# Kernel tuning notes

Measured on AMD Instinct MI355X. Metric: run time of the kernel, lower is better.

## Reference

```python
import jax, jax.numpy as jnp
import numpy as np

H = 8        # num_heads
LN_EPS = 1e-5
NEG = -1000000.0


def setup_inputs() -> dict:
    key = jax.random.key(0)
    ks = jax.random.split(key, 8)
    B, T, D = 4, 4096, 1024
    s = 1.0 / np.sqrt(D)
    x = jax.random.normal(ks[0], (B, T, D), dtype=jnp.float32)
    tmask = (jnp.arange(T) < (3 * T) // 4).astype(jnp.float32)
    src_mask = jnp.broadcast_to(tmask[None, :, None], (B, T, 1)).astype(jnp.float32)
    Wq = jax.random.normal(ks[1], (D, D), dtype=jnp.float32) * s
    Wk = jax.random.normal(ks[2], (D, D), dtype=jnp.float32) * s
    Wv = jax.random.normal(ks[3], (D, D), dtype=jnp.float32) * s
    bq = jnp.zeros((D,), jnp.float32)
    bk = jnp.zeros((D,), jnp.float32)
    bv = jnp.zeros((D,), jnp.float32)
    gamma = jnp.ones((D,), jnp.float32)
    beta = jnp.zeros((D,), jnp.float32)
    return {"x": x, "src_mask": src_mask, "Wq": Wq, "bq": bq, "Wk": Wk,
            "bk": bk, "Wv": Wv, "bv": bv, "gamma": gamma, "beta": beta}


def reference(x, src_mask, Wq, bq, Wk, bk, Wv, bv, gamma, beta):
    B, T, D = x.shape
    Dh = D // H
    # LayerNorm (same normed input feeds q, k, v)
    mu = jnp.mean(x, axis=-1, keepdims=True)
    var = jnp.mean(jnp.square(x - mu), axis=-1, keepdims=True)
    xn = (x - mu) * jax.lax.rsqrt(var + LN_EPS) * gamma + beta
    q = xn @ Wq + bq                               # [B,T,D]
    k = xn @ Wk + bk + (1.0 - src_mask) * NEG      # mask padded timesteps
    v = (xn @ Wv + bv) * src_mask                  # zero padded values
    q = jax.nn.softmax(q.reshape(B, T, H, Dh), axis=-1)   # over feature dim
    k = jax.nn.softmax(k.reshape(B, T, H, Dh), axis=1)    # over time dim
    v = v.reshape(B, T, H, Dh)
    # efficient/linear attention: O(T * Dh^2) per head
    att = jnp.einsum('bnhd,bnhl->bhdl', k, v)      # [B,H,Dh,Dh]
    y = jnp.einsum('bnhd,bhdl->bnhl', q, att).reshape(B, T, D)
    return x + y
```

## Files before the change

### kernel.cpp

```cpp
#include <hip/hip_runtime.h>
#include <stdint.h>


typedef unsigned short u16;
typedef __attribute__((ext_vector_type(8))) short bf16x8;
typedef __attribute__((ext_vector_type(4))) float f32x4;

__device__ u16 g_WT[3][1024 * 1024];
__device__ u16 g_xn[16777216];
__device__ u16 g_ekT[16777216];
__device__ u16 g_vvT[16777216];
__device__ float g_attp[8388608];
__device__ u16 g_attT[524288];
__device__ float g_Z[4096];

__device__ __forceinline__ float b2f(u16 u) {
  union { unsigned int i; float f; } c;
  c.i = ((unsigned int)u) << 16;
  return c.f;
}
__device__ __forceinline__ u16 f2b(float f) {
  union { float f; unsigned int i; } c;
  c.f = f;
  unsigned int r = c.i + 0x7fffu + ((c.i >> 16) & 1u);
  return (u16)(r >> 16);
}

__device__ __forceinline__ void gload16(const void* g, void* l) {
  __builtin_amdgcn_global_load_lds(
      reinterpret_cast<const __attribute__((address_space(1))) uint32_t*>(
          reinterpret_cast<uintptr_t>(g)),
      reinterpret_cast<__attribute__((address_space(3))) uint32_t*>(
          reinterpret_cast<uintptr_t>(l)),
      16, 0, 0);
}

__device__ __forceinline__ void stage128x32(const u16* g, int stride, char* lds,
                                            int wave, int lane) {
  const int r = wave * 32 + (lane >> 2);
  const int cb = (lane & 3) * 16;
  const char* gp = (const char*)g;
  gload16(gp + (size_t)r * stride * 2 + cb, lds + wave * 2048);
  gload16(gp + (size_t)(r + 16) * stride * 2 + cb, lds + wave * 2048 + 1024);
}

__device__ __forceinline__ bf16x8 frag_ld(const char* lds, int row, int lane) {
  return *(const bf16x8*)(lds + row * 64 + ((lane >> 4) * 16));
}

__global__ __launch_bounds__(256) void ln_kernel(const float* __restrict__ x,
                                                 const float* __restrict__ gamma,
                                                 const float* __restrict__ beta) {
  const int row = blockIdx.x;
  const int tid = threadIdx.x;
  const int wave = tid >> 6, lane = tid & 63;
  const float* xr = x + (size_t)row * 1024;
  float4 u = ((const float4*)xr)[tid];
  float v0 = u.x, v1 = u.y, v2 = u.z, v3 = u.w;
  float s = v0 + v1 + v2 + v3;
  float s2 = v0 * v0 + v1 * v1 + v2 * v2 + v3 * v3;
#pragma unroll
  for (int off = 32; off > 0; off >>= 1) {
    s += __shfl_down(s, off);
    s2 += __shfl_down(s2, off);
  }
  __shared__ float ls[4], ls2[4];
  if (lane == 0) { ls[wave] = s; ls2[wave] = s2; }
  __syncthreads();
  s = ls[0] + ls[1] + ls[2] + ls[3];
  s2 = ls2[0] + ls2[1] + ls2[2] + ls2[3];
  const float mu = s * (1.0f / 1024.0f);
  const float var = fmaxf(s2 * (1.0f / 1024.0f) - mu * mu, 0.0f);
  const float rstd = rsqrtf(var + 1e-5f);
  float4 g4 = ((const float4*)gamma)[tid];
  float4 be = ((const float4*)beta)[tid];
  ushort4 o;
  o.x = f2b((v0 - mu) * rstd * g4.x + be.x);
  o.y = f2b((v1 - mu) * rstd * g4.y + be.y);
  o.z = f2b((v2 - mu) * rstd * g4.z + be.z);
  o.w = f2b((v3 - mu) * rstd * g4.w + be.w);
  *(ushort4*)(g_xn + (size_t)row * 1024 + tid * 4) = o;
}

__global__ __launch_bounds__(256) void transpose_kernel(const float* __restrict__ wq,
                                                        const float* __restrict__ wk,
                                                        const float* __restrict__ wv) {
  __shared__ u16 tile[32][33];
  const int which = blockIdx.z;
  const float* src = (which == 0) ? wq : (which == 1) ? wk : wv;
  u16* dst = g_WT[which];
  const int tx = threadIdx.x & 31;
  const int ty = threadIdx.x >> 5;
  const int c0 = blockIdx.x * 32, r0 = blockIdx.y * 32;
#pragma unroll
  for (int i = 0; i < 4; i++)
    tile[ty + i * 8][tx] = f2b(src[(size_t)(r0 + ty + i * 8) * 1024 + c0 + tx]);
  __syncthreads();
#pragma unroll
  for (int i = 0; i < 4; i++)
    dst[(size_t)(c0 + ty + i * 8) * 1024 + r0 + tx] = tile[tx][ty + i * 8];
}

__global__ __launch_bounds__(256) void gemm_kv(const float* __restrict__ bk,
                                               const float* __restrict__ bv,
                                               const float* __restrict__ mask) {
  __shared__ __align__(16) char smem[34816];
  char* As = smem;
  char* Bs = smem + 8192;
  u16* tT = (u16*)smem;
  const int tid = threadIdx.x, wave = tid >> 6, lane = tid & 63;
  const int L = blockIdx.x;
  const int c = L & 7;
  const int k = L >> 3;
  const int inner = k & 15;
  const int n0 = (inner & 7) * 128;
  const int z = inner >> 3;
  const int m0 = (c + 8 * (k >> 4)) * 128;
  const u16* wt = z ? g_WT[2] : g_WT[1];
  const float* bias = z ? bv : bk;
  u16* outT = z ? g_vvT : g_ekT;
  const int b = m0 >> 12;
  const int t0 = m0 & 4095;
  const int wm = wave & 1, wn = wave >> 1;

  f32x4 zero = {0.f, 0.f, 0.f, 0.f};
  f32x4 acc[4][4];
#pragma unroll
  for (int i = 0; i < 4; i++)
#pragma unroll
    for (int j = 0; j < 4; j++) acc[i][j] = zero;

  for (int k0 = 0; k0 < 1024; k0 += 32) {
    __syncthreads();
    stage128x32(g_xn + (size_t)m0 * 1024 + k0, 1024, As, wave, lane);
    stage128x32(wt + (size_t)n0 * 1024 + k0, 1024, Bs, wave, lane);
    __syncthreads();
    bf16x8 af[4], bfr[4];
#pragma unroll
    for (int i = 0; i < 4; i++) af[i] = frag_ld(As, wm * 64 + i * 16 + (lane & 15), lane);
#pragma unroll
    for (int j = 0; j < 4; j++) bfr[j] = frag_ld(Bs, wn * 64 + j * 16 + (lane & 15), lane);
#pragma unroll
    for (int i = 0; i < 4; i++)
#pragma unroll
      for (int j = 0; j < 4; j++)
        acc[i][j] = __builtin_amdgcn_mfma_f32_16x16x32_bf16(af[i], bfr[j], acc[i][j], 0, 0, 0);
  }
  __syncthreads();

#pragma unroll
  for (int i = 0; i < 4; i++)
#pragma unroll
    for (int r = 0; r < 4; r++) {
      const int rowl = wm * 64 + i * 16 + (lane >> 4) * 4 + r;
      const float mv = mask[m0 + rowl];
#pragma unroll
      for (int j = 0; j < 4; j++) {
        const int coll = wn * 64 + j * 16 + (lane & 15);
        const float a = acc[i][j][r] + bias[n0 + coll];
        float o;
        if (z)
          o = a * mv;
        else
          o = (mv > 0.5f) ? __expf(fminf(a, 30.0f)) : 0.0f;
        tT[coll * 136 + rowl] = f2b(o);
      }
    }
  __syncthreads();
  const size_t gbase = (size_t)b * (1024 * 4096) + (size_t)n0 * 4096 + t0;
#pragma unroll
  for (int u = 0; u < 8; u++) {
    const int v = u * 256 + tid;
    const int cc = v >> 4, rb = (v & 15) * 8;
    uint4 val = *(const uint4*)&tT[cc * 136 + rb];
    *(uint4*)(outT + gbase + (size_t)cc * 4096 + rb) = val;
  }
}

__global__ __launch_bounds__(256) void zrow_kernel() {
  const int tid = threadIdx.x, wave = tid >> 6, lane = tid & 63;
  const int d = blockIdx.x * 4 + wave;
  const int b = blockIdx.y;
  const u16* p = g_ekT + (size_t)b * (1024 * 4096) + (size_t)d * 4096;
  float s = 0.f;
#pragma unroll
  for (int pass = 0; pass < 8; pass++) {
    uint4 w4 = *(const uint4*)(p + pass * 512 + lane * 8);
    unsigned int w[4] = {w4.x, w4.y, w4.z, w4.w};
#pragma unroll
    for (int q = 0; q < 4; q++) {
      s += b2f((u16)(w[q] & 0xffff));
      s += b2f((u16)(w[q] >> 16));
    }
  }
#pragma unroll
  for (int m = 1; m < 64; m <<= 1) s += __shfl_xor(s, m);
  if (lane == 0) g_Z[b * 1024 + d] = s;
}

__global__ __launch_bounds__(256) void gemm_att() {
  __shared__ __align__(16) char As[8192];
  __shared__ __align__(16) char Bs[8192];
  const int tid = threadIdx.x, wave = tid >> 6, lane = tid & 63;
  const int kc = blockIdx.x;
  const int bh = blockIdx.y;
  const int b = bh >> 3, h = bh & 7;
  const size_t base = (size_t)b * (1024 * 4096) + (size_t)(h * 128) * 4096;
  const int wm = wave & 1, wn = wave >> 1;

  f32x4 zero = {0.f, 0.f, 0.f, 0.f};
  f32x4 acc[4][4];
#pragma unroll
  for (int i = 0; i < 4; i++)
#pragma unroll
    for (int j = 0; j < 4; j++) acc[i][j] = zero;

  for (int kt = 0; kt < 256; kt += 32) {
    const int k0 = kc * 256 + kt;
    __syncthreads();
    stage128x32(g_ekT + base + k0, 4096, As, wave, lane);
    stage128x32(g_vvT + base + k0, 4096, Bs, wave, lane);
    __syncthreads();
    bf16x8 af[4], bfr[4];
#pragma unroll
    for (int i = 0; i < 4; i++) af[i] = frag_ld(As, wm * 64 + i * 16 + (lane & 15), lane);
#pragma unroll
    for (int j = 0; j < 4; j++) bfr[j] = frag_ld(Bs, wn * 64 + j * 16 + (lane & 15), lane);
#pragma unroll
    for (int i = 0; i < 4; i++)
#pragma unroll
      for (int j = 0; j < 4; j++)
        acc[i][j] = __builtin_amdgcn_mfma_f32_16x16x32_bf16(af[i], bfr[j], acc[i][j], 0, 0, 0);
  }

  float* op = g_attp + ((size_t)(kc * 32 + bh)) * 16384;
#pragma unroll
  for (int i = 0; i < 4; i++)
#pragma unroll
    for (int r = 0; r < 4; r++) {
      const int row = wm * 64 + i * 16 + (lane >> 4) * 4 + r;
#pragma unroll
      for (int j = 0; j < 4; j++) {
        const int col = wn * 64 + j * 16 + (lane & 15);
        op[row * 128 + col] = acc[i][j][r];
      }
    }
}

__global__ __launch_bounds__(256) void attnorm_kernel() {
  const int bh = blockIdx.x;
  const int b = bh >> 3, h = bh & 7;
  const int tid = threadIdx.x;
  __shared__ float Zl[128];
  if (tid < 128) Zl[tid] = fmaxf(g_Z[b * 1024 + h * 128 + tid], 1e-30f);
  __syncthreads();
  const int i0 = blockIdx.y * 2048;
  for (int i = i0 + tid; i < i0 + 2048; i += 256) {
    const int d = i >> 7, l = i & 127;
    float s = 0.f;
#pragma unroll
    for (int c = 0; c < 16; c++) s += g_attp[((size_t)(c * 32 + bh)) * 16384 + i];
    g_attT[(size_t)bh * 16384 + l * 128 + d] = f2b(s / Zl[d]);
  }
}

__global__ __launch_bounds__(256) void gemm_qy(const float* __restrict__ bq,
                                               const float* __restrict__ x,
                                               float* __restrict__ out) {
  __shared__ __align__(16) char As[8192];
  __shared__ __align__(16) char Bs[8192];
  __shared__ __align__(16) u16 qs[128 * 136];
  __shared__ float zqp[2][128];
  const int tid = threadIdx.x, wave = tid >> 6, lane = tid & 63;
  const int L = blockIdx.x;
  const int c = L & 7;
  const int k = L >> 3;
  const int h = k & 7;
  const int m0 = (c + 8 * (k >> 3)) * 128;
  const int b = m0 >> 12;
  const int bh = b * 8 + h;
  const int wm = wave & 1, wn = wave >> 1;

  f32x4 zero = {0.f, 0.f, 0.f, 0.f};
  f32x4 acc[4][4];
#pragma unroll
  for (int i = 0; i < 4; i++)
#pragma unroll
    for (int j = 0; j < 4; j++) acc[i][j] = zero;

  for (int k0 = 0; k0 < 1024; k0 += 32) {
    __syncthreads();
    stage128x32(g_xn + (size_t)m0 * 1024 + k0, 1024, As, wave, lane);
    stage128x32(g_WT[0] + (size_t)(h * 128) * 1024 + k0, 1024, Bs, wave, lane);
    __syncthreads();
    bf16x8 af[4], bfr[4];
#pragma unroll
    for (int i = 0; i < 4; i++) af[i] = frag_ld(As, wm * 64 + i * 16 + (lane & 15), lane);
#pragma unroll
    for (int j = 0; j < 4; j++) bfr[j] = frag_ld(Bs, wn * 64 + j * 16 + (lane & 15), lane);
#pragma unroll
    for (int i = 0; i < 4; i++)
#pragma unroll
      for (int j = 0; j < 4; j++)
        acc[i][j] = __builtin_amdgcn_mfma_f32_16x16x32_bf16(af[i], bfr[j], acc[i][j], 0, 0, 0);
  }

#pragma unroll
  for (int i = 0; i < 4; i++)
#pragma unroll
    for (int r = 0; r < 4; r++) {
      const int rowl = wm * 64 + i * 16 + (lane >> 4) * 4 + r;
      float rs = 0.f;
#pragma unroll
      for (int j = 0; j < 4; j++) {
        const int coll = wn * 64 + j * 16 + (lane & 15);
        const float e = __expf(fminf(acc[i][j][r] + bq[h * 128 + coll], 30.0f));
        qs[rowl * 136 + coll] = f2b(e);
        rs += e;
      }
      rs += __shfl_xor(rs, 1);
      rs += __shfl_xor(rs, 2);
      rs += __shfl_xor(rs, 4);
      rs += __shfl_xor(rs, 8);
      if ((lane & 15) == 0) zqp[wn][rowl] = rs;
    }
  __syncthreads();

  f32x4 acc2[4][4];
#pragma unroll
  for (int i = 0; i < 4; i++)
#pragma unroll
    for (int j = 0; j < 4; j++) acc2[i][j] = zero;

  for (int k0 = 0; k0 < 128; k0 += 32) {
    __syncthreads();
    stage128x32(g_attT + (size_t)bh * 16384 + k0, 128, Bs, wave, lane);
    __syncthreads();
    bf16x8 af[4], bfr[4];
#pragma unroll
    for (int i = 0; i < 4; i++)
      af[i] = *(const bf16x8*)&qs[(wm * 64 + i * 16 + (lane & 15)) * 136 + k0 + (lane >> 4) * 8];
#pragma unroll
    for (int j = 0; j < 4; j++) bfr[j] = frag_ld(Bs, wn * 64 + j * 16 + (lane & 15), lane);
#pragma unroll
    for (int i = 0; i < 4; i++)
#pragma unroll
      for (int j = 0; j < 4; j++)
        acc2[i][j] = __builtin_amdgcn_mfma_f32_16x16x32_bf16(af[i], bfr[j], acc2[i][j], 0, 0, 0);
  }

#pragma unroll
  for (int i = 0; i < 4; i++)
#pragma unroll
    for (int r = 0; r < 4; r++) {
      const int rowl = wm * 64 + i * 16 + (lane >> 4) * 4 + r;
      const float zq = fmaxf(zqp[0][rowl] + zqp[1][rowl], 1e-30f);
      const size_t n = (size_t)m0 + rowl;
#pragma unroll
      for (int j = 0; j < 4; j++) {
        const int coll = wn * 64 + j * 16 + (lane & 15);
        const size_t idx = n * 1024 + h * 128 + coll;
        out[idx] = x[idx] + acc2[i][j][r] / zq;
      }
    }
}

extern "C" void kernel_launch(void* const* d_in, const int* in_sizes, int n_in,
                              void* d_out, int out_size, void* d_ws, size_t ws_size,
                              hipStream_t stream) {
  const float* x = (const float*)d_in[0];
  const float* mask = (const float*)d_in[1];
  const float* Wq = (const float*)d_in[2];
  const float* bq = (const float*)d_in[3];
  const float* Wk = (const float*)d_in[4];
  const float* bk = (const float*)d_in[5];
  const float* Wv = (const float*)d_in[6];
  const float* bv = (const float*)d_in[7];
  const float* gamma = (const float*)d_in[8];
  const float* beta = (const float*)d_in[9];
  float* out = (float*)d_out;
  (void)d_ws; (void)ws_size;

  transpose_kernel<<<dim3(32, 32, 3), 256, 0, stream>>>(Wq, Wk, Wv);
  ln_kernel<<<dim3(16384), 256, 0, stream>>>(x, gamma, beta);
  gemm_kv<<<dim3(2048), 256, 0, stream>>>(bk, bv, mask);
  zrow_kernel<<<dim3(256, 4), 256, 0, stream>>>();
  gemm_att<<<dim3(16, 32), 256, 0, stream>>>();
  attnorm_kernel<<<dim3(32, 8), 256, 0, stream>>>();
  gemm_qy<<<dim3(1024), 256, 0, stream>>>(bq, x, out);
}
```

Baseline: 380.1 us.

## Double-buffer GEMM LDS staging, merge LN with transpose, fuse Z sums into gemm_kv

```diff
diff --git a/kernel.cpp b/kernel.cpp
--- a/kernel.cpp
+++ b/kernel.cpp
@@ -48,65 +48,86 @@
   return *(const bf16x8*)(lds + row * 64 + ((lane >> 4) * 16));
 }
 
-__global__ __launch_bounds__(256) void ln_kernel(const float* __restrict__ x,
-                                                 const float* __restrict__ gamma,
-                                                 const float* __restrict__ beta) {
-  const int row = blockIdx.x;
+__device__ __forceinline__ void tile_mfma(const char* As, const char* Bs,
+                                          f32x4 (&acc)[4][4], int wm, int wn,
+                                          int lane) {
+  bf16x8 af[4], bfr[4];
+#pragma unroll
+  for (int i = 0; i < 4; i++) af[i] = frag_ld(As, wm * 64 + i * 16 + (lane & 15), lane);
+#pragma unroll
+  for (int j = 0; j < 4; j++) bfr[j] = frag_ld(Bs, wn * 64 + j * 16 + (lane & 15), lane);
+#pragma unroll
+  for (int i = 0; i < 4; i++)
+#pragma unroll
+    for (int j = 0; j < 4; j++)
+      acc[i][j] = __builtin_amdgcn_mfma_f32_16x16x32_bf16(af[i], bfr[j], acc[i][j], 0, 0, 0);
+}
+
+__global__ __launch_bounds__(256) void prep_kernel(const float* __restrict__ x,
+                                                   const float* __restrict__ gamma,
+                                                   const float* __restrict__ beta,
+                                                   const float* __restrict__ wq,
+                                                   const float* __restrict__ wk,
+                                                   const float* __restrict__ wv) {
+  __shared__ float ls[4], ls2[4];
+  __shared__ u16 tile[32][33];
+  const int bid = blockIdx.x;
   const int tid = threadIdx.x;
-  const int wave = tid >> 6, lane = tid & 63;
-  const float* xr = x + (size_t)row * 1024;
-  float4 u = ((const float4*)xr)[tid];
-  float v0 = u.x, v1 = u.y, v2 = u.z, v3 = u.w;
-  float s = v0 + v1 + v2 + v3;
-  float s2 = v0 * v0 + v1 * v1 + v2 * v2 + v3 * v3;
-#pragma unroll
-  for (int off = 32; off > 0; off >>= 1) {
-    s += __shfl_down(s, off);
-    s2 += __shfl_down(s2, off);
-  }
-  __shared__ float ls[4], ls2[4];
-  if (lane == 0) { ls[wave] = s; ls2[wave] = s2; }
-  __syncthreads();
-  s = ls[0] + ls[1] + ls[2] + ls[3];
-  s2 = ls2[0] + ls2[1] + ls2[2] + ls2[3];
-  const float mu = s * (1.0f / 1024.0f);
-  const float var = fmaxf(s2 * (1.0f / 1024.0f) - mu * mu, 0.0f);
-  const float rstd = rsqrtf(var + 1e-5f);
-  float4 g4 = ((const float4*)gamma)[tid];
-  float4 be = ((const float4*)beta)[tid];
-  ushort4 o;
-  o.x = f2b((v0 - mu) * rstd * g4.x + be.x);
-  o.y = f2b((v1 - mu) * rstd * g4.y + be.y);
-  o.z = f2b((v2 - mu) * rstd * g4.z + be.z);
-  o.w = f2b((v3 - mu) * rstd * g4.w + be.w);
-  *(ushort4*)(g_xn + (size_t)row * 1024 + tid * 4) = o;
-}
-
-__global__ __launch_bounds__(256) void transpose_kernel(const float* __restrict__ wq,
-                                                        const float* __restrict__ wk,
-                                                        const float* __restrict__ wv) {
-  __shared__ u16 tile[32][33];
-  const int which = blockIdx.z;
-  const float* src = (which == 0) ? wq : (which == 1) ? wk : wv;
-  u16* dst = g_WT[which];
-  const int tx = threadIdx.x & 31;
-  const int ty = threadIdx.x >> 5;
-  const int c0 = blockIdx.x * 32, r0 = blockIdx.y * 32;
-#pragma unroll
-  for (int i = 0; i < 4; i++)
-    tile[ty + i * 8][tx] = f2b(src[(size_t)(r0 + ty + i * 8) * 1024 + c0 + tx]);
-  __syncthreads();
-#pragma unroll
-  for (int i = 0; i < 4; i++)
-    dst[(size_t)(c0 + ty + i * 8) * 1024 + r0 + tx] = tile[tx][ty + i * 8];
+  if (bid < 16384) {
+    if (bid < 16) g_Z[bid * 256 + tid] = 0.0f;
+    const int wave = tid >> 6, lane = tid & 63;
+    const float* xr = x + (size_t)bid * 1024;
+    float4 u = ((const float4*)xr)[tid];
+    float v0 = u.x, v1 = u.y, v2 = u.z, v3 = u.w;
+    float s = v0 + v1 + v2 + v3;
+    float s2 = v0 * v0 + v1 * v1 + v2 * v2 + v3 * v3;
+#pragma unroll
+    for (int off = 32; off > 0; off >>= 1) {
+      s += __shfl_down(s, off);
+      s2 += __shfl_down(s2, off);
+    }
+    if (lane == 0) { ls[wave] = s; ls2[wave] = s2; }
+    __syncthreads();
+    s = ls[0] + ls[1] + ls[2] + ls[3];
+    s2 = ls2[0] + ls2[1] + ls2[2] + ls2[3];
+    const float mu = s * (1.0f / 1024.0f);
+    const float var = fmaxf(s2 * (1.0f / 1024.0f) - mu * mu, 0.0f);
+    const float rstd = rsqrtf(var + 1e-5f);
+    float4 g4 = ((const float4*)gamma)[tid];
+    float4 be = ((const float4*)beta)[tid];
+    ushort4 o;
+    o.x = f2b((v0 - mu) * rstd * g4.x + be.x);
+    o.y = f2b((v1 - mu) * rstd * g4.y + be.y);
+    o.z = f2b((v2 - mu) * rstd * g4.z + be.z);
+    o.w = f2b((v3 - mu) * rstd * g4.w + be.w);
+    *(ushort4*)(g_xn + (size_t)bid * 1024 + tid * 4) = o;
+  } else {
+    const int id = bid - 16384;
+    const int which = id >> 10;
+    const int rem = id & 1023;
+    const float* src = (which == 0) ? wq : (which == 1) ? wk : wv;
+    u16* dst = g_WT[which];
+    const int tx = tid & 31;
+    const int ty = tid >> 5;
+    const int c0 = (rem & 31) * 32, r0 = (rem >> 5) * 32;
+#pragma unroll
+    for (int i = 0; i < 4; i++)
+      tile[ty + i * 8][tx] = f2b(src[(size_t)(r0 + ty + i * 8) * 1024 + c0 + tx]);
+    __syncthreads();
+#pragma unroll
+    for (int i = 0; i < 4; i++)
+      dst[(size_t)(c0 + ty + i * 8) * 1024 + r0 + tx] = tile[tx][ty + i * 8];
+  }
 }
 
 __global__ __launch_bounds__(256) void gemm_kv(const float* __restrict__ bk,
                                                const float* __restrict__ bv,
                                                const float* __restrict__ mask) {
   __shared__ __align__(16) char smem[34816];
-  char* As = smem;
-  char* Bs = smem + 8192;
+  char* A0 = smem;
+  char* B0 = smem + 8192;
+  char* A1 = smem + 16384;
+  char* B1 = smem + 24576;
   u16* tT = (u16*)smem;
   const int tid = threadIdx.x, wave = tid >> 6, lane = tid & 63;
   const int L = blockIdx.x;
@@ -122,6 +143,8 @@
   const int b = m0 >> 12;
   const int t0 = m0 & 4095;
   const int wm = wave & 1, wn = wave >> 1;
+  const u16* Ag = g_xn + (size_t)m0 * 1024;
+  const u16* Bg = wt + (size_t)n0 * 1024;
 
   f32x4 zero = {0.f, 0.f, 0.f, 0.f};
   f32x4 acc[4][4];
@@ -130,24 +153,23 @@
 #pragma unroll
     for (int j = 0; j < 4; j++) acc[i][j] = zero;
 
-  for (int k0 = 0; k0 < 1024; k0 += 32) {
-    __syncthreads();
-    stage128x32(g_xn + (size_t)m0 * 1024 + k0, 1024, As, wave, lane);
-    stage128x32(wt + (size_t)n0 * 1024 + k0, 1024, Bs, wave, lane);
-    __syncthreads();
-    bf16x8 af[4], bfr[4];
-#pragma unroll
-    for (int i = 0; i < 4; i++) af[i] = frag_ld(As, wm * 64 + i * 16 + (lane & 15), lane);
-#pragma unroll
-    for (int j = 0; j < 4; j++) bfr[j] = frag_ld(Bs, wn * 64 + j * 16 + (lane & 15), lane);
-#pragma unroll
-    for (int i = 0; i < 4; i++)
-#pragma unroll
-      for (int j = 0; j < 4; j++)
-        acc[i][j] = __builtin_amdgcn_mfma_f32_16x16x32_bf16(af[i], bfr[j], acc[i][j], 0, 0, 0);
-  }
-  __syncthreads();
-
+  stage128x32(Ag, 1024, A0, wave, lane);
+  stage128x32(Bg, 1024, B0, wave, lane);
+  __syncthreads();
+  for (int k0 = 0; k0 < 1024; k0 += 64) {
+    stage128x32(Ag + k0 + 32, 1024, A1, wave, lane);
+    stage128x32(Bg + k0 + 32, 1024, B1, wave, lane);
+    tile_mfma(A0, B0, acc, wm, wn, lane);
+    __syncthreads();
+    if (k0 + 64 < 1024) {
+      stage128x32(Ag + k0 + 64, 1024, A0, wave, lane);
+      stage128x32(Bg + k0 + 64, 1024, B0, wave, lane);
+    }
+    tile_mfma(A1, B1, acc, wm, wn, lane);
+    __syncthreads();
+  }
+
+  float fsum[4] = {0.f, 0.f, 0.f, 0.f};
 #pragma unroll
   for (int i = 0; i < 4; i++)
 #pragma unroll
@@ -163,9 +185,20 @@
           o = a * mv;
         else
           o = (mv > 0.5f) ? __expf(fminf(a, 30.0f)) : 0.0f;
-        tT[coll * 136 + rowl] = f2b(o);
+        const u16 ob = f2b(o);
+        tT[coll * 136 + rowl] = ob;
+        if (!z) fsum[j] += b2f(ob);
       }
     }
+  if (!z) {
+#pragma unroll
+    for (int j = 0; j < 4; j++) {
+      float s = fsum[j];
+      s += __shfl_xor(s, 16);
+      s += __shfl_xor(s, 32);
+      if (lane < 16) atomicAdd(&g_Z[b * 1024 + n0 + wn * 64 + j * 16 + lane], s);
+    }
+  }
   __syncthreads();
   const size_t gbase = (size_t)b * (1024 * 4096) + (size_t)n0 * 4096 + t0;
 #pragma unroll
@@ -177,36 +210,20 @@
   }
 }
 
-__global__ __launch_bounds__(256) void zrow_kernel() {
-  const int tid = threadIdx.x, wave = tid >> 6, lane = tid & 63;
-  const int d = blockIdx.x * 4 + wave;
-  const int b = blockIdx.y;
-  const u16* p = g_ekT + (size_t)b * (1024 * 4096) + (size_t)d * 4096;
-  float s = 0.f;
-#pragma unroll
-  for (int pass = 0; pass < 8; pass++) {
-    uint4 w4 = *(const uint4*)(p + pass * 512 + lane * 8);
-    unsigned int w[4] = {w4.x, w4.y, w4.z, w4.w};
-#pragma unroll
-    for (int q = 0; q < 4; q++) {
-      s += b2f((u16)(w[q] & 0xffff));
-      s += b2f((u16)(w[q] >> 16));
-    }
-  }
-#pragma unroll
-  for (int m = 1; m < 64; m <<= 1) s += __shfl_xor(s, m);
-  if (lane == 0) g_Z[b * 1024 + d] = s;
-}
-
 __global__ __launch_bounds__(256) void gemm_att() {
-  __shared__ __align__(16) char As[8192];
-  __shared__ __align__(16) char Bs[8192];
+  __shared__ __align__(16) char smem[32768];
+  char* A0 = smem;
+  char* B0 = smem + 8192;
+  char* A1 = smem + 16384;
+  char* B1 = smem + 24576;
   const int tid = threadIdx.x, wave = tid >> 6, lane = tid & 63;
   const int kc = blockIdx.x;
   const int bh = blockIdx.y;
   const int b = bh >> 3, h = bh & 7;
   const size_t base = (size_t)b * (1024 * 4096) + (size_t)(h * 128) * 4096;
   const int wm = wave & 1, wn = wave >> 1;
+  const u16* Ag = g_ekT + base + kc * 256;
+  const u16* Bg = g_vvT + base + kc * 256;
 
   f32x4 zero = {0.f, 0.f, 0.f, 0.f};
   f32x4 acc[4][4];
@@ -215,22 +232,20 @@
 #pragma unroll
     for (int j = 0; j < 4; j++) acc[i][j] = zero;
 
-  for (int kt = 0; kt < 256; kt += 32) {
-    const int k0 = kc * 256 + kt;
-    __syncthreads();
-    stage128x32(g_ekT + base + k0, 4096, As, wave, lane);
-    stage128x32(g_vvT + base + k0, 4096, Bs, wave, lane);
-    __syncthreads();
-    bf16x8 af[4], bfr[4];
-#pragma unroll
-    for (int i = 0; i < 4; i++) af[i] = frag_ld(As, wm * 64 + i * 16 + (lane & 15), lane);
-#pragma unroll
-    for (int j = 0; j < 4; j++) bfr[j] = frag_ld(Bs, wn * 64 + j * 16 + (lane & 15), lane);
-#pragma unroll
-    for (int i = 0; i < 4; i++)
-#pragma unroll
-      for (int j = 0; j < 4; j++)
-        acc[i][j] = __builtin_amdgcn_mfma_f32_16x16x32_bf16(af[i], bfr[j], acc[i][j], 0, 0, 0);
+  stage128x32(Ag, 4096, A0, wave, lane);
+  stage128x32(Bg, 4096, B0, wave, lane);
+  __syncthreads();
+  for (int kt = 0; kt < 256; kt += 64) {
+    stage128x32(Ag + kt + 32, 4096, A1, wave, lane);
+    stage128x32(Bg + kt + 32, 4096, B1, wave, lane);
+    tile_mfma(A0, B0, acc, wm, wn, lane);
+    __syncthreads();
+    if (kt + 64 < 256) {
+      stage128x32(Ag + kt + 64, 4096, A0, wave, lane);
+      stage128x32(Bg + kt + 64, 4096, B0, wave, lane);
+    }
+    tile_mfma(A1, B1, acc, wm, wn, lane);
+    __syncthreads();
   }
 
   float* op = g_attp + ((size_t)(kc * 32 + bh)) * 16384;
@@ -267,10 +282,15 @@
 __global__ __launch_bounds__(256) void gemm_qy(const float* __restrict__ bq,
                                                const float* __restrict__ x,
                                                float* __restrict__ out) {
-  __shared__ __align__(16) char As[8192];
-  __shared__ __align__(16) char Bs[8192];
-  __shared__ __align__(16) u16 qs[128 * 136];
+  __shared__ __align__(16) char smem[51200];
   __shared__ float zqp[2][128];
+  char* A0 = smem;
+  char* B0 = smem + 8192;
+  char* A1 = smem + 16384;
+  char* B1 = smem + 24576;
+  u16* qs = (u16*)smem;
+  char* C0 = smem + 34816;
+  char* C1 = smem + 43008;
   const int tid = threadIdx.x, wave = tid >> 6, lane = tid & 63;
   const int L = blockIdx.x;
   const int c = L & 7;
@@ -280,6 +300,9 @@
   const int b = m0 >> 12;
   const int bh = b * 8 + h;
   const int wm = wave & 1, wn = wave >> 1;
+  const u16* Ag = g_xn + (size_t)m0 * 1024;
+  const u16* Bg = g_WT[0] + (size_t)(h * 128) * 1024;
+  const u16* Cg = g_attT + (size_t)bh * 16384;
 
   f32x4 zero = {0.f, 0.f, 0.f, 0.f};
   f32x4 acc[4][4];
@@ -288,22 +311,23 @@
 #pragma unroll
     for (int j = 0; j < 4; j++) acc[i][j] = zero;
 
-  for (int k0 = 0; k0 < 1024; k0 += 32) {
-    __syncthreads();
-    stage128x32(g_xn + (size_t)m0 * 1024 + k0, 1024, As, wave, lane);
-    stage128x32(g_WT[0] + (size_t)(h * 128) * 1024 + k0, 1024, Bs, wave, lane);
-    __syncthreads();
-    bf16x8 af[4], bfr[4];
-#pragma unroll
-    for (int i = 0; i < 4; i++) af[i] = frag_ld(As, wm * 64 + i * 16 + (lane & 15), lane);
-#pragma unroll
-    for (int j = 0; j < 4; j++) bfr[j] = frag_ld(Bs, wn * 64 + j * 16 + (lane & 15), lane);
-#pragma unroll
-    for (int i = 0; i < 4; i++)
-#pragma unroll
-      for (int j = 0; j < 4; j++)
-        acc[i][j] = __builtin_amdgcn_mfma_f32_16x16x32_bf16(af[i], bfr[j], acc[i][j], 0, 0, 0);
-  }
+  stage128x32(Ag, 1024, A0, wave, lane);
+  stage128x32(Bg, 1024, B0, wave, lane);
+  __syncthreads();
+  for (int k0 = 0; k0 < 1024; k0 += 64) {
+    stage128x32(Ag + k0 + 32, 1024, A1, wave, lane);
+    stage128x32(Bg + k0 + 32, 1024, B1, wave, lane);
+    tile_mfma(A0, B0, acc, wm, wn, lane);
+    __syncthreads();
+    if (k0 + 64 < 1024) {
+      stage128x32(Ag + k0 + 64, 1024, A0, wave, lane);
+      stage128x32(Bg + k0 + 64, 1024, B0, wave, lane);
+    }
+    tile_mfma(A1, B1, acc, wm, wn, lane);
+    __syncthreads();
+  }
+
+  stage128x32(Cg, 128, C0, wave, lane);
 
 #pragma unroll
   for (int i = 0; i < 4; i++)
@@ -332,21 +356,37 @@
 #pragma unroll
     for (int j = 0; j < 4; j++) acc2[i][j] = zero;
 
-  for (int k0 = 0; k0 < 128; k0 += 32) {
-    __syncthreads();
-    stage128x32(g_attT + (size_t)bh * 16384 + k0, 128, Bs, wave, lane);
-    __syncthreads();
-    bf16x8 af[4], bfr[4];
-#pragma unroll
-    for (int i = 0; i < 4; i++)
-      af[i] = *(const bf16x8*)&qs[(wm * 64 + i * 16 + (lane & 15)) * 136 + k0 + (lane >> 4) * 8];
-#pragma unroll
-    for (int j = 0; j < 4; j++) bfr[j] = frag_ld(Bs, wn * 64 + j * 16 + (lane & 15), lane);
-#pragma unroll
-    for (int i = 0; i < 4; i++)
-#pragma unroll
-      for (int j = 0; j < 4; j++)
-        acc2[i][j] = __builtin_amdgcn_mfma_f32_16x16x32_bf16(af[i], bfr[j], acc2[i][j], 0, 0, 0);
+  for (int k0 = 0; k0 < 128; k0 += 64) {
+    stage128x32(Cg + k0 + 32, 128, C1, wave, lane);
+    {
+      bf16x8 af[4], bfr[4];
+#pragma unroll
+      for (int i = 0; i < 4; i++)
+        af[i] = *(const bf16x8*)&qs[(wm * 64 + i * 16 + (lane & 15)) * 136 + k0 + (lane >> 4) * 8];
+#pragma unroll
+      for (int j = 0; j < 4; j++) bfr[j] = frag_ld(C0, wn * 64 + j * 16 + (lane & 15), lane);
+#pragma unroll
+      for (int i = 0; i < 4; i++)
+#pragma unroll
+        for (int j = 0; j < 4; j++)
+          acc2[i][j] = __builtin_amdgcn_mfma_f32_16x16x32_bf16(af[i], bfr[j], acc2[i][j], 0, 0, 0);
+    }
+    __syncthreads();
+    if (k0 + 64 < 128) stage128x32(Cg + k0 + 64, 128, C0, wave, lane);
+    {
+      bf16x8 af[4], bfr[4];
+#pragma unroll
+      for (int i = 0; i < 4; i++)
+        af[i] = *(const bf16x8*)&qs[(wm * 64 + i * 16 + (lane & 15)) * 136 + k0 + 32 + (lane >> 4) * 8];
+#pragma unroll
+      for (int j = 0; j < 4; j++) bfr[j] = frag_ld(C1, wn * 64 + j * 16 + (lane & 15), lane);
+#pragma unroll
+      for (int i = 0; i < 4; i++)
+#pragma unroll
+        for (int j = 0; j < 4; j++)
+          acc2[i][j] = __builtin_amdgcn_mfma_f32_16x16x32_bf16(af[i], bfr[j], acc2[i][j], 0, 0, 0);
+    }
+    __syncthreads();
   }
 
 #pragma unroll
@@ -381,10 +421,8 @@
   float* out = (float*)d_out;
   (void)d_ws; (void)ws_size;
 
-  transpose_kernel<<<dim3(32, 32, 3), 256, 0, stream>>>(Wq, Wk, Wv);
-  ln_kernel<<<dim3(16384), 256, 0, stream>>>(x, gamma, beta);
+  prep_kernel<<<dim3(16384 + 3072), 256, 0, stream>>>(x, gamma, beta, Wq, Wk, Wv);
   gemm_kv<<<dim3(2048), 256, 0, stream>>>(bk, bv, mask);
-  zrow_kernel<<<dim3(256, 4), 256, 0, stream>>>();
   gemm_att<<<dim3(16, 32), 256, 0, stream>>>();
   attnorm_kernel<<<dim3(32, 8), 256, 0, stream>>>();
   gemm_qy<<<dim3(1024), 256, 0, stream>>>(bq, x, out);
```

New measurement: 378.0 us. About the same (-0.6%).
